# Kernel optimization log

Hardware: AMD Instinct MI355X
Metric: run time of the kernel (lower is better)

## Reference

```python
import jax, jax.numpy as jnp
import numpy as np

NUM_NODES = 100000
NUM_EDGES = 400000
EPS = 1e-9


def _find(parent, u):
    # chase parent pointers to the root (no path compression; parent is
    # immutable within one find, so this terminates because union-by-rank
    # keeps the forest acyclic)
    return jax.lax.while_loop(lambda v: parent[v] != v, lambda v: parent[v], u)


def _kruskal(scores, edge_index, num_nodes):
    """Greedy Kruskal over edges sorted by descending score, via union-find.
    Returns b in {0,1}^E with exactly (num_nodes-1) ones if the graph is
    connected (fewer otherwise), identical acceptance set to the torch loop."""
    E = scores.shape[0]
    order = jnp.argsort(-scores)  # descending
    src = edge_index[0].astype(jnp.int32)
    dst = edge_index[1].astype(jnp.int32)
    max_used = jnp.int32(num_nodes - 1)

    def step(carry, idx):
        parent, rank, b, used = carry
        i = src[idx]
        j = dst[idx]
        ru = _find(parent, i)
        rv = _find(parent, j)
        accept = (ru != rv) & (used < max_used)
        ri = rank[ru]
        rj = rank[rv]
        # union by rank: if ri<rj attach ru under rv, else attach rv under ru;
        # if ranks equal, root ru gains rank (matches the torch union())
        child = jnp.where(ri < rj, ru, rv)
        root = jnp.where(ri < rj, rv, ru)
        parent = parent.at[child].set(jnp.where(accept, root, parent[child]))
        rank = rank.at[root].add(jnp.where(accept & (ri == rj), jnp.int32(1), jnp.int32(0)))
        b = b.at[idx].set(accept.astype(b.dtype))
        used = used + accept.astype(used.dtype)
        return (parent, rank, b, used), None

    parent0 = jnp.arange(num_nodes, dtype=jnp.int32)
    rank0 = jnp.zeros(num_nodes, dtype=jnp.int32)
    b0 = jnp.zeros(E, dtype=scores.dtype)
    (parent, rank, b, used), _ = jax.lax.scan(step, (parent0, rank0, b0, jnp.int32(0)), order)
    return b


def setup_inputs() -> dict:
    key = jax.random.key(0)
    k1, k2, k3 = jax.random.split(key, 3)
    s = jax.random.normal(k1, (NUM_EDGES,), dtype=jnp.float32)
    u = jax.random.uniform(k2, (NUM_EDGES,), dtype=jnp.float32)
    edge_index = jax.random.randint(k3, (2, NUM_EDGES), 0, NUM_NODES, dtype=jnp.int32)
    return {"s": s, "u": u, "edge_index": edge_index, "num_nodes": NUM_NODES}


def reference(s, u, edge_index, num_nodes):
    s_prob = jax.nn.sigmoid(s)
    gumbel = -jnp.log(-jnp.log(u + EPS) + EPS)
    scores = s_prob + gumbel
    return _kruskal(scores, edge_index, num_nodes)
```

## Files before the change

kernel.cpp:

```cpp
#include <hip/hip_runtime.h>
#include <stdint.h>

#define V_NODES 100000
#define MAX_ROUNDS 13
#define TB 256
#define RPT 4
#define TBL 2048
#define TBL_FROM 3

struct alignas(16) Rec { unsigned long long k; unsigned int a, b; };

__device__ __forceinline__ unsigned long long make_key(float sv, float uv, int id) {
    float sp = 1.0f / (1.0f + expf(-sv));
    float g  = -logf(-logf(uv + 1e-9f) + 1e-9f);
    unsigned int b = __float_as_uint(sp + g);
    unsigned int m = (b & 0x80000000u) ? ~b : (b | 0x80000000u);
    return ((unsigned long long)(~m) << 19) | (unsigned long long)(unsigned)id;
}

__device__ __forceinline__ int find_root(const int* __restrict__ parent, int v) {
    int p = parent[v];
    int pp = parent[p];
    while (p != pp) { p = pp; pp = parent[p]; }
    return p;
}

__device__ __forceinline__ void gbid(unsigned long long* __restrict__ best,
                                     unsigned int* __restrict__ guess,
                                     unsigned int root, unsigned long long k) {
    unsigned int kh = (unsigned int)(k >> 32);
    unsigned int g = guess[root];
    if (kh > g) return;
    if (kh < g) guess[root] = kh;
    atomicMin(&best[root], k);
}

__global__ void k_scan0(const float* __restrict__ s, const float* __restrict__ u,
                        const int* __restrict__ src, const int* __restrict__ dst,
                        float* __restrict__ out, unsigned long long* __restrict__ best,
                        unsigned int* __restrict__ guess,
                        Rec* __restrict__ recs, int* __restrict__ parent,
                        int* __restrict__ flags, int E) {
    int e = blockIdx.x * blockDim.x + threadIdx.x;
    if (e >= E) return;
    if (e < V_NODES) parent[e] = e;
    if (e < MAX_ROUNDS) flags[e] = (e == 0) ? 1 : 0;
    unsigned int a = src[e], b = dst[e];
    Rec r;
    r.k = make_key(s[e], u[e], e);
    r.a = a; r.b = b;
    recs[e] = r;
    out[e] = 0.0f;
    if (a != b) {
        gbid(best, guess, a, r.k);
        gbid(best, guess, b, r.k);
    }
}

__global__ void k_scan(const int* __restrict__ parent,
                       unsigned long long* __restrict__ bestC,
                       unsigned int* __restrict__ guess,
                       Rec* __restrict__ recs, int* __restrict__ flags,
                       int r, int E) {
    __shared__ int sflag;
    __shared__ unsigned int tag[TBL];
    __shared__ unsigned long long tkey[TBL];
    if (flags[r - 1] == 0) return;
    const bool useTbl = (r >= TBL_FROM);
    if (useTbl)
        for (int t = threadIdx.x; t < TBL; t += TB) { tag[t] = 0xFFFFFFFFu; tkey[t] = ~0ULL; }
    if (threadIdx.x == 0) sflag = 0;
    __syncthreads();

    int base = (blockIdx.x * blockDim.x + threadIdx.x) * RPT;
    bool cross = false;

    Rec rec[RPT];
    int pa[RPT], pb[RPT];
    bool live[RPT];
    #pragma unroll
    for (int j = 0; j < RPT; ++j) {
        int i = base + j;
        if (i < E) rec[j] = recs[i];
        else { rec[j].a = 0; rec[j].b = 0; }
        live[j] = (rec[j].a != rec[j].b);
    }
    #pragma unroll
    for (int j = 0; j < RPT; ++j)
        if (live[j]) { pa[j] = parent[rec[j].a]; pb[j] = parent[rec[j].b]; }

    auto bid = [&](unsigned int root, unsigned long long k) {
        if (useTbl) {
            unsigned int s1 = root & (TBL - 1);
            unsigned int prev = atomicCAS(&tag[s1], 0xFFFFFFFFu, root);
            if (prev == 0xFFFFFFFFu || prev == root) {
                atomicMin(&tkey[s1], k);
                return;
            }
            unsigned int s2 = (root * 2654435761u >> 19) & (TBL - 1);
            prev = atomicCAS(&tag[s2], 0xFFFFFFFFu, root);
            if (prev == 0xFFFFFFFFu || prev == root) {
                atomicMin(&tkey[s2], k);
                return;
            }
        }
        gbid(bestC, guess, root, k);
    };

    #pragma unroll
    for (int j = 0; j < RPT; ++j) {
        if (!live[j]) continue;
        int i = base + j;
        int ra = pa[j], rb = pb[j];
        int p = parent[ra]; while (ra != p) { ra = p; p = parent[ra]; }
        p = parent[rb];     while (rb != p) { rb = p; p = parent[rb]; }
        if (ra == rb) {
            *(uint2*)&recs[i].a = make_uint2((unsigned)ra, (unsigned)ra);
        } else {
            cross = true;
            if ((unsigned)ra != rec[j].a || (unsigned)rb != rec[j].b)
                *(uint2*)&recs[i].a = make_uint2((unsigned)ra, (unsigned)rb);
            bid((unsigned)ra, rec[j].k);
            bid((unsigned)rb, rec[j].k);
        }
    }
    if (cross) sflag = 1;
    __syncthreads();

    if (useTbl)
        for (int t = threadIdx.x; t < TBL; t += TB) {
            unsigned int rt = tag[t];
            if (rt != 0xFFFFFFFFu) gbid(bestC, guess, rt, tkey[t]);
        }
    if (threadIdx.x == 0 && sflag) flags[r] = 1;
}

__global__ void k_choose(const int* __restrict__ src, const int* __restrict__ dst,
                         int* __restrict__ parent,
                         const unsigned long long* __restrict__ bestC,
                         float* __restrict__ out, const int* __restrict__ flags,
                         int r) {
    if (flags[r] == 0) return;
    int v = blockIdx.x * blockDim.x + threadIdx.x;
    if (v >= V_NODES) return;
    unsigned long long k = bestC[v];
    if ((unsigned)(k >> 51) != 0u) return;
    int id = (int)(unsigned int)(k & 0x7FFFFu);
    int a0 = src[id], b0 = dst[id];
    int ru = find_root(parent, a0);
    int rv = find_root(parent, b0);
    if (ru != a0) parent[a0] = ru;
    if (rv != b0) parent[b0] = rv;
    int other = (ru == v) ? rv : ru;
    out[id] = 1.0f;
    if (bestC[other] != k || v > other) {
        if (other != v) parent[v] = other;
    }
}

extern "C" void kernel_launch(void* const* d_in, const int* in_sizes, int n_in,
                              void* d_out, int out_size, void* d_ws, size_t ws_size,
                              hipStream_t stream) {
    const float* s  = (const float*)d_in[0];
    const float* u  = (const float*)d_in[1];
    const int*   ei = (const int*)d_in[2];
    const int E = in_sizes[0];
    const int* src = ei;
    const int* dst = ei + E;
    float* out = (float*)d_out;

    char* ws = (char*)d_ws;
    Rec* recs = (Rec*)ws;
    unsigned long long* bestAll = (unsigned long long*)(recs + E);
    int* parent = (int*)(bestAll + (size_t)MAX_ROUNDS * V_NODES);
    unsigned int* guessAll = (unsigned int*)(parent + V_NODES);
    int* flags  = (int*)(guessAll + (size_t)MAX_ROUNDS * V_NODES);

    const int gE  = (E + TB - 1) / TB;
    const int gE4 = (E + TB * RPT - 1) / (TB * RPT);
    const int gV  = (V_NODES + TB - 1) / TB;

    k_scan0<<<gE, TB, 0, stream>>>(s, u, src, dst, out, bestAll, guessAll,
                                   recs, parent, flags, E);
    k_choose<<<gV, TB, 0, stream>>>(src, dst, parent, bestAll, out, flags, 0);

    for (int r = 1; r < MAX_ROUNDS; ++r) {
        unsigned long long* best_r = bestAll + (size_t)r * V_NODES;
        unsigned int* guess_r = guessAll + (size_t)r * V_NODES;
        k_scan<<<gE4, TB, 0, stream>>>(parent, best_r, guess_r, recs, flags, r, E);
        k_choose<<<gV, TB, 0, stream>>>(src, dst, parent, best_r, out, flags, r);
    }
}
```

Baseline: 272.7 us.

## Compact live cross-component edges into ping-pong buffers each Boruvka round

Each scan round now stream-compacts the still-live edges, those whose endpoints have different roots, into a second record buffer using wave ballot and atomic offsets. Later rounds read only those edges and exit blocks beyond the live count. The per-round flag array is replaced by per-round live counts. This cuts the memory traffic and find work of late rounds on edges already inside one component, at the cost of atomics and scattered writes for compaction and a second buffer of edge records in the workspace.

```diff
diff --git a/kernel.cpp b/kernel.cpp
--- a/kernel.cpp
+++ b/kernel.cpp
@@ -40,11 +40,11 @@
                         float* __restrict__ out, unsigned long long* __restrict__ best,
                         unsigned int* __restrict__ guess,
                         Rec* __restrict__ recs, int* __restrict__ parent,
-                        int* __restrict__ flags, int E) {
+                        int* __restrict__ counts, int E) {
     int e = blockIdx.x * blockDim.x + threadIdx.x;
     if (e >= E) return;
     if (e < V_NODES) parent[e] = e;
-    if (e < MAX_ROUNDS) flags[e] = (e == 0) ? 1 : 0;
+    if (e <= MAX_ROUNDS) counts[e] = (e == 1) ? E : 0;
     unsigned int a = src[e], b = dst[e];
     Rec r;
     r.k = make_key(s[e], u[e], e);
@@ -60,34 +60,35 @@
 __global__ void k_scan(const int* __restrict__ parent,
                        unsigned long long* __restrict__ bestC,
                        unsigned int* __restrict__ guess,
-                       Rec* __restrict__ recs, int* __restrict__ flags,
-                       int r, int E) {
-    __shared__ int sflag;
+                       const Rec* __restrict__ recsIn,
+                       Rec* __restrict__ recsOut,
+                       int* __restrict__ counts, int r) {
     __shared__ unsigned int tag[TBL];
     __shared__ unsigned long long tkey[TBL];
-    if (flags[r - 1] == 0) return;
+    const int n = counts[r];
+    if (n == 0) return;
+    if (blockIdx.x * (TB * RPT) >= n) return;
     const bool useTbl = (r >= TBL_FROM);
-    if (useTbl)
+    if (useTbl) {
         for (int t = threadIdx.x; t < TBL; t += TB) { tag[t] = 0xFFFFFFFFu; tkey[t] = ~0ULL; }
-    if (threadIdx.x == 0) sflag = 0;
-    __syncthreads();
-
-    int base = (blockIdx.x * blockDim.x + threadIdx.x) * RPT;
-    bool cross = false;
+        __syncthreads();
+    }
+
+    int base = (blockIdx.x * TB + threadIdx.x) * RPT;
 
     Rec rec[RPT];
-    int pa[RPT], pb[RPT];
+    int ra[RPT], rb[RPT];
     bool live[RPT];
     #pragma unroll
     for (int j = 0; j < RPT; ++j) {
         int i = base + j;
-        if (i < E) rec[j] = recs[i];
-        else { rec[j].a = 0; rec[j].b = 0; }
+        if (i < n) rec[j] = recsIn[i];
+        else { rec[j].k = 0; rec[j].a = 0; rec[j].b = 0; }
         live[j] = (rec[j].a != rec[j].b);
     }
     #pragma unroll
     for (int j = 0; j < RPT; ++j)
-        if (live[j]) { pa[j] = parent[rec[j].a]; pb[j] = parent[rec[j].b]; }
+        if (live[j]) { ra[j] = parent[rec[j].a]; rb[j] = parent[rec[j].b]; }
 
     auto bid = [&](unsigned int root, unsigned long long k) {
         if (useTbl) {
@@ -110,37 +111,46 @@
     #pragma unroll
     for (int j = 0; j < RPT; ++j) {
         if (!live[j]) continue;
-        int i = base + j;
-        int ra = pa[j], rb = pb[j];
-        int p = parent[ra]; while (ra != p) { ra = p; p = parent[ra]; }
-        p = parent[rb];     while (rb != p) { rb = p; p = parent[rb]; }
-        if (ra == rb) {
-            *(uint2*)&recs[i].a = make_uint2((unsigned)ra, (unsigned)ra);
-        } else {
-            cross = true;
-            if ((unsigned)ra != rec[j].a || (unsigned)rb != rec[j].b)
-                *(uint2*)&recs[i].a = make_uint2((unsigned)ra, (unsigned)rb);
-            bid((unsigned)ra, rec[j].k);
-            bid((unsigned)rb, rec[j].k);
-        }
-    }
-    if (cross) sflag = 1;
-    __syncthreads();
-
-    if (useTbl)
+        int x = ra[j]; int p = parent[x]; while (x != p) { x = p; p = parent[x]; } ra[j] = x;
+        x = rb[j];     p = parent[x]; while (x != p) { x = p; p = parent[x]; } rb[j] = x;
+        live[j] = (ra[j] != rb[j]);
+        if (live[j]) {
+            bid((unsigned)ra[j], rec[j].k);
+            bid((unsigned)rb[j], rec[j].k);
+        }
+    }
+
+    int lane = threadIdx.x & 63;
+    #pragma unroll
+    for (int j = 0; j < RPT; ++j) {
+        unsigned long long mask = __ballot(live[j]);
+        if (mask == 0) continue;
+        int leader = __ffsll((long long)mask) - 1;
+        int pos = 0;
+        if (lane == leader) pos = atomicAdd(&counts[r + 1], (int)__popcll(mask));
+        pos = __shfl(pos, leader);
+        if (live[j]) {
+            int my = pos + (int)__popcll(mask & ((1ull << lane) - 1ull));
+            Rec o; o.k = rec[j].k; o.a = (unsigned)ra[j]; o.b = (unsigned)rb[j];
+            recsOut[my] = o;
+        }
+    }
+
+    if (useTbl) {
+        __syncthreads();
         for (int t = threadIdx.x; t < TBL; t += TB) {
             unsigned int rt = tag[t];
             if (rt != 0xFFFFFFFFu) gbid(bestC, guess, rt, tkey[t]);
         }
-    if (threadIdx.x == 0 && sflag) flags[r] = 1;
+    }
 }
 
 __global__ void k_choose(const int* __restrict__ src, const int* __restrict__ dst,
                          int* __restrict__ parent,
                          const unsigned long long* __restrict__ bestC,
-                         float* __restrict__ out, const int* __restrict__ flags,
+                         float* __restrict__ out, const int* __restrict__ counts,
                          int r) {
-    if (flags[r] == 0) return;
+    if (counts[r + 1] == 0) return;
     int v = blockIdx.x * blockDim.x + threadIdx.x;
     if (v >= V_NODES) return;
     unsigned long long k = bestC[v];
@@ -170,24 +180,28 @@
     float* out = (float*)d_out;
 
     char* ws = (char*)d_ws;
-    Rec* recs = (Rec*)ws;
-    unsigned long long* bestAll = (unsigned long long*)(recs + E);
+    Rec* recsA = (Rec*)ws;
+    Rec* recsB = recsA + E;
+    unsigned long long* bestAll = (unsigned long long*)(recsB + E);
     int* parent = (int*)(bestAll + (size_t)MAX_ROUNDS * V_NODES);
     unsigned int* guessAll = (unsigned int*)(parent + V_NODES);
-    int* flags  = (int*)(guessAll + (size_t)MAX_ROUNDS * V_NODES);
+    int* counts = (int*)(guessAll + (size_t)MAX_ROUNDS * V_NODES);
 
     const int gE  = (E + TB - 1) / TB;
     const int gE4 = (E + TB * RPT - 1) / (TB * RPT);
     const int gV  = (V_NODES + TB - 1) / TB;
 
     k_scan0<<<gE, TB, 0, stream>>>(s, u, src, dst, out, bestAll, guessAll,
-                                   recs, parent, flags, E);
-    k_choose<<<gV, TB, 0, stream>>>(src, dst, parent, bestAll, out, flags, 0);
+                                   recsA, parent, counts, E);
+    k_choose<<<gV, TB, 0, stream>>>(src, dst, parent, bestAll, out, counts, 0);
 
     for (int r = 1; r < MAX_ROUNDS; ++r) {
         unsigned long long* best_r = bestAll + (size_t)r * V_NODES;
         unsigned int* guess_r = guessAll + (size_t)r * V_NODES;
-        k_scan<<<gE4, TB, 0, stream>>>(parent, best_r, guess_r, recs, flags, r, E);
-        k_choose<<<gV, TB, 0, stream>>>(src, dst, parent, best_r, out, flags, r);
-    }
-}
+        const Rec* rin = (r & 1) ? recsA : recsB;
+        Rec* rout      = (r & 1) ? recsB : recsA;
+        k_scan<<<gE4, TB, 0, stream>>>(parent, best_r, guess_r, rin, rout,
+                                       counts, r);
+        k_choose<<<gV, TB, 0, stream>>>(src, dst, parent, best_r, out, counts, r);
+    }
+}
```

Result: slower. 579.2 us (+112.4%).
